# Optimization experiments

Measured on AMD Instinct MI355X. Metric: run time of the kernel, lower is better.

## Reference

```python
import jax, jax.numpy as jnp
import numpy as np

B, N, C = 8, 2048, 256
DK, DV = 64, 256


def setup_inputs() -> dict:
    key = jax.random.key(0)
    kx, kq, kk, kv = jax.random.split(key, 4)
    x = jax.random.normal(kx, (B, N, C), dtype=jnp.float32)
    # Conv1d(kernel=1, bias=False) weights: [out_channels, in_channels]
    Wq = jax.random.normal(kq, (DK, C), dtype=jnp.float32) * (1.0 / np.sqrt(C))
    Wk = jax.random.normal(kk, (DK, C), dtype=jnp.float32) * (1.0 / np.sqrt(C))
    Wv = jax.random.normal(kv, (DV, C), dtype=jnp.float32) * (1.0 / np.sqrt(C))
    return {"x": x, "Wq": Wq, "Wk": Wk, "Wv": Wv}


def reference(x, Wq, Wk, Wv):
    # kernel-size-1 conv == per-point linear projection
    q = jnp.einsum('bnc,dc->bnd', x, Wq)   # [B, N, dk]
    k = jnp.einsum('bnc,dc->bnd', x, Wk)   # [B, N, dk]
    v = jnp.einsum('bnc,dc->bnd', x, Wv)   # [B, N, dv]
    energy = jnp.einsum('bnd,bmd->bnm', q, k)  # [B, N, N] == bmm(q, k^T)
    # offset-attention branch: softmax over dim=1 (column-wise),
    # then renormalize each row to sum to 1
    attention = jax.nn.softmax(energy, axis=1)
    attention = attention / (1e-9 + attention.sum(axis=-1, keepdims=True))
    x_r = jnp.einsum('bnm,bmd->bnd', attention, v)  # [B, N, dv]
    return x_r
```

## Files before the change

### kernel.cpp

```cpp
#include <hip/hip_runtime.h>
#include <hip/hip_bf16.h>

#define BB 8
#define NN 2048
#define CC 256
#define DKK 64
#define DVV 256
#define COFF 60.0f

typedef __attribute__((ext_vector_type(8))) short bf16x8;
typedef __attribute__((ext_vector_type(4))) float f32x4;

#define MFMA16 __builtin_amdgcn_mfma_f32_16x16x32_bf16

static __device__ __forceinline__ unsigned short f2bf(float f) {
    unsigned int u = __float_as_uint(f);
    u += 0x7fffu + ((u >> 16) & 1u);
    return (unsigned short)(u >> 16);
}
static __device__ __forceinline__ float bf2f(unsigned short h) {
    return __uint_as_float(((unsigned int)h) << 16);
}

static __device__ __forceinline__ void g2l16(const unsigned short* g, unsigned short* l) {
    __builtin_amdgcn_global_load_lds(
        (const __attribute__((address_space(1))) void*)g,
        (__attribute__((address_space(3))) void*)l, 16, 0, 0);
}

__global__ void k_wt(const float* __restrict__ Wq, const float* __restrict__ Wk,
                     const float* __restrict__ Wv,
                     unsigned short* __restrict__ Wqkh_s, unsigned short* __restrict__ Wqkl_s,
                     unsigned short* __restrict__ Wvs) {
    int idx = blockIdx.x * 256 + threadIdx.x;
    if (idx >= 384 * 256) return;
    int d = idx >> 8, c = idx & 255;
    float w;
    if (d < 64)       w = Wq[d * 256 + c];
    else if (d < 128) w = Wk[(d - 64) * 256 + c];
    else              w = Wv[(d - 128) * 256 + c];
    unsigned short h = f2bf(w);
    int c8 = c >> 3;
    if (d < 128) {
        int row = d;
        int csw = (((c8 & 24) | ((c8 ^ row) & 7)) << 3) | (c & 7);
        Wqkh_s[row * 256 + csw] = h;
        Wqkl_s[row * 256 + csw] = f2bf(w - bf2f(h));
    } else {
        int row = d - 128;
        int csw = (((c8 & 24) | ((c8 ^ row) & 7)) << 3) | (c & 7);
        Wvs[row * 256 + csw] = h;
    }
}

__global__ __launch_bounds__(256) void k_split(
    const float* __restrict__ x,
    unsigned short* __restrict__ xh, unsigned short* __restrict__ xl) {
    int tid = blockIdx.x * 256 + threadIdx.x;
    const float4* xp = (const float4*)x + tid * 2;
    float4 a = xp[0], b = xp[1];
    float v[8] = {a.x, a.y, a.z, a.w, b.x, b.y, b.z, b.w};
    ushort4 h4[2], l4[2];
    #pragma unroll
    for (int i = 0; i < 8; ++i) {
        unsigned short h = f2bf(v[i]);
        ((unsigned short*)h4)[i] = h;
        ((unsigned short*)l4)[i] = f2bf(v[i] - bf2f(h));
    }
    ((ushort4*)xh)[tid * 2]     = h4[0];
    ((ushort4*)xh)[tid * 2 + 1] = h4[1];
    ((ushort4*)xl)[tid * 2]     = l4[0];
    ((ushort4*)xl)[tid * 2 + 1] = l4[1];
}

__global__ __launch_bounds__(1024) void k_vproj(
    const unsigned short* __restrict__ xh, const unsigned short* __restrict__ Wvs,
    unsigned short* __restrict__ vT)
{
    __shared__ __align__(16) unsigned short Wlds[256 * 256];
    int tid = threadIdx.x;
    int w = tid >> 6, lane = tid & 63;
    int t = lane & 15, qd = lane >> 4;
    int i = w >> 2, j = w & 3;
    int bn0 = blockIdx.x * 64;

    {
        int lr = lane >> 5, lc = (lane & 31) << 3;
        #pragma unroll
        for (int s = 0; s < 8; ++s) {
            int r0 = (w * 8 + s) * 2;
            g2l16(Wvs + (size_t)(r0 + lr) * 256 + lc, &Wlds[0] + (size_t)r0 * 256);
        }
    }

    int bn = bn0 + i * 16 + t;
    int b = bn >> 11, n = bn & 2047;
    bf16x8 bfr[8];
    const unsigned short* bp = xh + (size_t)bn * 256 + qd * 8;
    #pragma unroll
    for (int c = 0; c < 8; ++c) bfr[c] = *(const bf16x8*)(bp + c * 32);

    __syncthreads();

    f32x4 acc[4];
    #pragma unroll
    for (int k = 0; k < 4; ++k) acc[k] = (f32x4){0.f, 0.f, 0.f, 0.f};
    #pragma unroll
    for (int c = 0; c < 8; ++c) {
        #pragma unroll
        for (int k = 0; k < 4; ++k) {
            int d = j * 64 + k * 16 + t;
            int c8 = c * 4 + qd;
            int pos = d * 256 + ((((c8 & 24) | ((c8 ^ t) & 7))) << 3);
            bf16x8 a = *(const bf16x8*)(&Wlds[pos]);
            acc[k] = MFMA16(a, bfr[c], acc[k], 0, 0, 0);
        }
    }
    #pragma unroll
    for (int k = 0; k < 4; ++k) {
        #pragma unroll
        for (int r = 0; r < 4; ++r) {
            int dvd = j * 64 + k * 16 + qd * 4 + r;
            int nsw = (n & ~63) | ((((n >> 3) ^ dvd) & 7) << 3) | (n & 7);
            vT[((size_t)b * 256 + dvd) * 2048 + nsw] = f2bf(acc[k][r]);
        }
    }
}

__global__ __launch_bounds__(1024) void k_qkproj(
    const unsigned short* __restrict__ xh, const unsigned short* __restrict__ xl,
    const unsigned short* __restrict__ Wqkh_s, const unsigned short* __restrict__ Wqkl_s,
    unsigned short* __restrict__ qh, unsigned short* __restrict__ ql,
    unsigned short* __restrict__ kh, unsigned short* __restrict__ kl)
{
    __shared__ __align__(16) unsigned short Wlds[2][128 * 256];
    int tid = threadIdx.x;
    int w = tid >> 6, lane = tid & 63;
    int t = lane & 15, qd = lane >> 4;
    int i = w >> 2, j = w & 3;
    int bn0 = blockIdx.x * 64;

    {
        int lr = lane >> 5, lc = (lane & 31) << 3;
        #pragma unroll
        for (int s = 0; s < 8; ++s) {
            int id = w * 8 + s;
            int plane = id >> 6;
            int r0 = (id & 63) * 2;
            const unsigned short* src = (plane ? Wqkl_s : Wqkh_s) + (size_t)(r0 + lr) * 256 + lc;
            g2l16(src, &Wlds[plane][0] + (size_t)r0 * 256);
        }
    }

    int bn = bn0 + i * 16 + t;
    bf16x8 bh[8], bl[8];
    const unsigned short* bph = xh + (size_t)bn * 256 + qd * 8;
    const unsigned short* bpl = xl + (size_t)bn * 256 + qd * 8;
    #pragma unroll
    for (int c = 0; c < 8; ++c) {
        bh[c] = *(const bf16x8*)(bph + c * 32);
        bl[c] = *(const bf16x8*)(bpl + c * 32);
    }

    __syncthreads();

    f32x4 acc[2];
    acc[0] = (f32x4){0.f, 0.f, 0.f, 0.f};
    acc[1] = (f32x4){0.f, 0.f, 0.f, 0.f};
    #pragma unroll
    for (int c = 0; c < 8; ++c) {
        #pragma unroll
        for (int k = 0; k < 2; ++k) {
            int d = j * 32 + k * 16 + t;
            int c8 = c * 4 + qd;
            int pos = d * 256 + ((((c8 & 24) | ((c8 ^ t) & 7))) << 3);
            bf16x8 ah = *(const bf16x8*)(&Wlds[0][pos]);
            bf16x8 al = *(const bf16x8*)(&Wlds[1][pos]);
            acc[k] = MFMA16(ah, bh[c], acc[k], 0, 0, 0);
            acc[k] = MFMA16(ah, bl[c], acc[k], 0, 0, 0);
            acc[k] = MFMA16(al, bh[c], acc[k], 0, 0, 0);
        }
    }
    #pragma unroll
    for (int k = 0; k < 2; ++k) {
        ushort4 h4, l4;
        #pragma unroll
        for (int r = 0; r < 4; ++r) {
            unsigned short h = f2bf(acc[k][r]);
            ((unsigned short*)&h4)[r] = h;
            ((unsigned short*)&l4)[r] = f2bf(acc[k][r] - bf2f(h));
        }
        int dbase = j * 32 + k * 16 + qd * 4;
        int dd = dbase & 63;
        int sw = ((((dd >> 3) ^ bn) & 7) << 3) | (dd & 7);
        if (dbase < 64) {
            *(ushort4*)(qh + (size_t)bn * 64 + sw) = h4;
            *(ushort4*)(ql + (size_t)bn * 64 + sw) = l4;
        } else {
            *(ushort4*)(kh + (size_t)bn * 64 + sw) = h4;
            *(ushort4*)(kl + (size_t)bn * 64 + sw) = l4;
        }
    }
}

__global__ __launch_bounds__(1024) void k_colsum(
    const unsigned short* __restrict__ qh, const unsigned short* __restrict__ ql,
    const unsigned short* __restrict__ kh, const unsigned short* __restrict__ kl,
    float* __restrict__ cs)
{
    __shared__ __align__(16) unsigned short qbuf[2][2][64 * 64];
    __shared__ float csbuf[4][64];
    int tid = threadIdx.x;
    int w = tid >> 6, lane = tid & 63;
    int t = lane & 15, qd = lane >> 4;
    int b = blockIdx.y, m0 = blockIdx.x * 64;
    int i = w >> 2, j = w & 3;

    int arow = m0 + i * 16 + t;
    int off0 = ((qd ^ (t & 7)) << 3);
    const unsigned short* kbh = kh + ((size_t)b * 2048 + arow) * 64;
    const unsigned short* kbl = kl + ((size_t)b * 2048 + arow) * 64;
    bf16x8 ah0 = *(const bf16x8*)(kbh + off0);
    bf16x8 ah1 = *(const bf16x8*)(kbh + (off0 ^ 32));
    bf16x8 al0 = *(const bf16x8*)(kbl + off0);
    bf16x8 al1 = *(const bf16x8*)(kbl + (off0 ^ 32));

    int lr = lane >> 3, lc = (lane & 7) << 3;
    const unsigned short* qsrc = ((w < 8) ? qh : ql) +
        ((size_t)b * 2048 + (w & 7) * 8 + lr) * 64 + lc;
    unsigned short* qdst = &qbuf[0][w >> 3][(w & 7) * 8 * 64];

#define STAGEQ(bufi, itv) g2l16(qsrc + (size_t)(itv) * (64 * 64), qdst + (bufi) * (2 * 64 * 64))

    float ssum[4] = {0.f, 0.f, 0.f, 0.f};
    STAGEQ(0, 0);
    for (int it = 0; it < 32; ++it) {
        __syncthreads();
        if (it + 1 < 32) STAGEQ((it + 1) & 1, it + 1);
        int cur = it & 1;
        int brow = j * 16 + t;
        const unsigned short* qrh = &qbuf[cur][0][brow * 64];
        const unsigned short* qrl = &qbuf[cur][1][brow * 64];
        bf16x8 bh0 = *(const bf16x8*)(qrh + off0);
        bf16x8 bh1 = *(const bf16x8*)(qrh + (off0 ^ 32));
        bf16x8 bl0 = *(const bf16x8*)(qrl + off0);
        bf16x8 bl1 = *(const bf16x8*)(qrl + (off0 ^ 32));
        f32x4 a0 = {0.f,0.f,0.f,0.f}, a1 = {0.f,0.f,0.f,0.f};
        a0 = MFMA16(ah0, bh0, a0, 0, 0, 0);
        a0 = MFMA16(ah1, bh1, a0, 0, 0, 0);
        a1 = MFMA16(ah0, bl0, a1, 0, 0, 0);
        a1 = MFMA16(ah1, bl1, a1, 0, 0, 0);
        a1 = MFMA16(al0, bh0, a1, 0, 0, 0);
        a1 = MFMA16(al1, bh1, a1, 0, 0, 0);
        #pragma unroll
        for (int r = 0; r < 4; ++r)
            ssum[r] += __expf((a0[r] + a1[r]) - COFF);
    }
#undef STAGEQ

    #pragma unroll
    for (int r = 0; r < 4; ++r) {
        float v = ssum[r];
        v += __shfl_xor(v, 1, 16);
        v += __shfl_xor(v, 2, 16);
        v += __shfl_xor(v, 4, 16);
        v += __shfl_xor(v, 8, 16);
        ssum[r] = v;
    }
    if (t == 0) {
        #pragma unroll
        for (int r = 0; r < 4; ++r) csbuf[j][i * 16 + qd * 4 + r] = ssum[r];
    }
    __syncthreads();
    if (tid < 64)
        cs[(size_t)b * 2048 + m0 + tid] =
            csbuf[0][tid] + csbuf[1][tid] + csbuf[2][tid] + csbuf[3][tid];
}

__global__ __launch_bounds__(1024) void k_attn(
    const unsigned short* __restrict__ qh, const unsigned short* __restrict__ ql,
    const unsigned short* __restrict__ kh, const unsigned short* __restrict__ kl,
    const unsigned short* __restrict__ vT, const float* __restrict__ cs,
    float* __restrict__ out)
{
    __shared__ __align__(16) unsigned short kbuf[2][128 * 64];
    __shared__ __align__(16) unsigned short vbuf[2][256 * 64];
    __shared__ __align__(16) unsigned short pP[64 * 72];
    __shared__ float cs_s[2048];
    __shared__ float rsbuf[4][64];

    int tid = threadIdx.x;
    int w = tid >> 6, lane = tid & 63;
    int t = lane & 15, qd = lane >> 4;
    int b = blockIdx.y;
    int n0 = blockIdx.x * 64;
    int i = w >> 2, j = w & 3;
    int i2 = w >> 3, j8 = w & 7;

    for (int u = tid; u < 2048; u += 1024) cs_s[u] = cs[(size_t)b * 2048 + u];

    int arow_a = n0 + i * 16 + t;
    int offq = ((qd ^ (t & 7)) << 3);
    const unsigned short* qbh = qh + ((size_t)b * 2048 + arow_a) * 64;
    const unsigned short* qbl = ql + ((size_t)b * 2048 + arow_a) * 64;
    bf16x8 ah0 = *(const bf16x8*)(qbh + offq);
    bf16x8 ah1 = *(const bf16x8*)(qbh + (offq ^ 32));
    bf16x8 al0 = *(const bf16x8*)(qbl + offq);
    bf16x8 al1 = *(const bf16x8*)(qbl + (offq ^ 32));

    int lr = lane >> 3, lc = (lane & 7) << 3;
    const unsigned short* vsrc0 = vT + ((size_t)b * 256 + w * 16 + lr) * 2048 + lc;
    const unsigned short* vsrc1 = vT + ((size_t)b * 256 + w * 16 + 8 + lr) * 2048 + lc;
    const unsigned short* karr = (w < 8) ? kh : kl;
    const unsigned short* ksrc = karr + ((size_t)b * 2048 + (w & 7) * 8 + lr) * 64 + lc;
    unsigned short* vdst0 = &vbuf[0][0] + w * 1024;
    unsigned short* vdst1 = vdst0 + 512;
    unsigned short* kdst = &kbuf[0][0] + w * 512;

#define STAGE(bufi, m0s) do { \
        g2l16(vsrc0 + (m0s), vdst0 + (bufi) * 16384); \
        g2l16(vsrc1 + (m0s), vdst1 + (bufi) * 16384); \
        g2l16(ksrc + (size_t)(m0s) * 64, kdst + (bufi) * 8192); \
    } while (0)

    f32x4 accv[2][2];
    accv[0][0] = (f32x4){0.f,0.f,0.f,0.f}; accv[0][1] = (f32x4){0.f,0.f,0.f,0.f};
    accv[1][0] = (f32x4){0.f,0.f,0.f,0.f}; accv[1][1] = (f32x4){0.f,0.f,0.f,0.f};
    float rs[4] = {0.f, 0.f, 0.f, 0.f};

    STAGE(0, 0);

    for (int it = 0; it < 32; ++it) {
        __syncthreads();
        int cur = it & 1;
        int m0 = it * 64;
        {
            int mr = j * 16 + t;
            int off0 = ((qd ^ (t & 7)) << 3);
            const unsigned short* khrow = &kbuf[cur][mr * 64];
            const unsigned short* klrow = &kbuf[cur][(64 + mr) * 64];
            bf16x8 bh0 = *(const bf16x8*)(khrow + off0);
            bf16x8 bh1 = *(const bf16x8*)(khrow + (off0 ^ 32));
            bf16x8 bl0 = *(const bf16x8*)(klrow + off0);
            bf16x8 bl1 = *(const bf16x8*)(klrow + (off0 ^ 32));
            f32x4 s0 = {0.f,0.f,0.f,0.f}, s1 = {0.f,0.f,0.f,0.f};
            s0 = MFMA16(ah0, bh0, s0, 0, 0, 0);
            s0 = MFMA16(ah1, bh1, s0, 0, 0, 0);
            s1 = MFMA16(ah0, bl0, s1, 0, 0, 0);
            s1 = MFMA16(ah1, bl1, s1, 0, 0, 0);
            s1 = MFMA16(al0, bh0, s1, 0, 0, 0);
            s1 = MFMA16(al1, bh1, s1, 0, 0, 0);
            float rcs = 1.0f / cs_s[m0 + j * 16 + t];
            unsigned short* prow = pP + (size_t)(i * 16 + qd * 4) * 72 + j * 16 + t;
            #pragma unroll
            for (int r = 0; r < 4; ++r) {
                float p = __expf((s0[r] + s1[r]) - COFF) * rcs;
                rs[r] += p;
                prow[r * 72] = f2bf(p);
            }
        }
        if (it + 1 < 32) STAGE((it + 1) & 1, m0 + 64);
        __syncthreads();
        {
            const unsigned short* vb = &vbuf[cur][0];
            #pragma unroll
            for (int c = 0; c < 2; ++c) {
                bf16x8 pa0 = *(const bf16x8*)(pP + (size_t)((2*i2 + 0) * 16 + t) * 72 + c * 32 + qd * 8);
                bf16x8 pa1 = *(const bf16x8*)(pP + (size_t)((2*i2 + 1) * 16 + t) * 72 + c * 32 + qd * 8);
                int ch = (((c * 4 + qd) ^ (t & 7)) << 3);
                bf16x8 vb0 = *(const bf16x8*)(vb + ((2*j8 + 0) * 16 + t) * 64 + ch);
                bf16x8 vb1 = *(const bf16x8*)(vb + ((2*j8 + 1) * 16 + t) * 64 + ch);
                accv[0][0] = MFMA16(pa0, vb0, accv[0][0], 0, 0, 0);
                accv[0][1] = MFMA16(pa0, vb1, accv[0][1], 0, 0, 0);
                accv[1][0] = MFMA16(pa1, vb0, accv[1][0], 0, 0, 0);
                accv[1][1] = MFMA16(pa1, vb1, accv[1][1], 0, 0, 0);
            }
        }
    }
#undef STAGE

    #pragma unroll
    for (int r = 0; r < 4; ++r) {
        float v = rs[r];
        v += __shfl_xor(v, 1, 16);
        v += __shfl_xor(v, 2, 16);
        v += __shfl_xor(v, 4, 16);
        v += __shfl_xor(v, 8, 16);
        rs[r] = v;
    }
    if (t == 0) {
        #pragma unroll
        for (int r = 0; r < 4; ++r) rsbuf[j][i * 16 + qd * 4 + r] = rs[r];
    }
    __syncthreads();

    #pragma unroll
    for (int s2 = 0; s2 < 2; ++s2) {
        #pragma unroll
        for (int r = 0; r < 4; ++r) {
            int nl = (2 * i2 + s2) * 16 + qd * 4 + r;
            float tot = rsbuf[0][nl] + rsbuf[1][nl] + rsbuf[2][nl] + rsbuf[3][nl];
            float sc = 1.0f / (1e-9f + tot);
            size_t orow = ((size_t)b * 2048 + n0 + nl) * 256;
            out[orow + (2 * j8 + 0) * 16 + t] = accv[s2][0][r] * sc;
            out[orow + (2 * j8 + 1) * 16 + t] = accv[s2][1][r] * sc;
        }
    }
}

extern "C" void kernel_launch(void* const* d_in, const int* in_sizes, int n_in,
                              void* d_out, int out_size, void* d_ws, size_t ws_size,
                              hipStream_t stream) {
    (void)in_sizes; (void)n_in; (void)out_size; (void)ws_size;
    const float* x  = (const float*)d_in[0];
    const float* Wq = (const float*)d_in[1];
    const float* Wk = (const float*)d_in[2];
    const float* Wv = (const float*)d_in[3];
    float* out = (float*)d_out;

    char* ws = (char*)d_ws;
    size_t off = 0;
    unsigned short* Wqkh_s = (unsigned short*)(ws + off); off += (size_t)128 * 256 * 2;
    unsigned short* Wqkl_s = (unsigned short*)(ws + off); off += (size_t)128 * 256 * 2;
    unsigned short* Wvs    = (unsigned short*)(ws + off); off += (size_t)256 * 256 * 2;
    unsigned short* xh = (unsigned short*)(ws + off); off += (size_t)BB * NN * CC * 2;
    unsigned short* xl = (unsigned short*)(ws + off); off += (size_t)BB * NN * CC * 2;
    unsigned short* qh = (unsigned short*)(ws + off); off += (size_t)BB * NN * DKK * 2;
    unsigned short* ql = (unsigned short*)(ws + off); off += (size_t)BB * NN * DKK * 2;
    unsigned short* kh = (unsigned short*)(ws + off); off += (size_t)BB * NN * DKK * 2;
    unsigned short* kl = (unsigned short*)(ws + off); off += (size_t)BB * NN * DKK * 2;
    unsigned short* vT = (unsigned short*)(ws + off); off += (size_t)BB * DVV * NN * 2;
    float* cs = (float*)(ws + off);                   off += (size_t)BB * NN * 4;

    hipLaunchKernelGGL(k_wt,     dim3(384),         dim3(256),  0, stream, Wq, Wk, Wv, Wqkh_s, Wqkl_s, Wvs);
    hipLaunchKernelGGL(k_split,  dim3(2048),        dim3(256),  0, stream, x, xh, xl);
    hipLaunchKernelGGL(k_vproj,  dim3(256),         dim3(1024), 0, stream, xh, Wvs, vT);
    hipLaunchKernelGGL(k_qkproj, dim3(256),         dim3(1024), 0, stream, xh, xl, Wqkh_s, Wqkl_s, qh, ql, kh, kl);
    hipLaunchKernelGGL(k_colsum, dim3(NN / 64, BB), dim3(1024), 0, stream, qh, ql, kh, kl, cs);
    hipLaunchKernelGGL(k_attn,   dim3(NN / 64, BB), dim3(1024), 0, stream, qh, ql, kh, kl, vT, cs, out);
}
```

Baseline: 167.5 us.

## Fuse x split and Q/K/V projections into one kernel, prefetch attention stage earlier

Removes the separate x hi/lo split kernel and merges the V and QK projection kernels into one launch with two roles chosen by blockIdx.y. Each block converts fp32 x to bf16 hi/lo in registers, so the xh/xl workspace round trip and two launches go away. In the attention kernel, the next tile's async stage is issued before the QK/softmax compute instead of after it, giving more overlap. In exchange, V blocks now also read fp32 x and compute an unused lo split, and the earlier prefetch depends on the buffer sync order still being correct.

Result: slower. 205.5 us (+22.7%).

```diff
diff --git a/kernel.cpp b/kernel.cpp
--- a/kernel.cpp
+++ b/kernel.cpp
@@ -53,28 +53,12 @@
     }
 }
 
-__global__ __launch_bounds__(256) void k_split(
+__global__ __launch_bounds__(1024) void k_proj(
     const float* __restrict__ x,
-    unsigned short* __restrict__ xh, unsigned short* __restrict__ xl) {
-    int tid = blockIdx.x * 256 + threadIdx.x;
-    const float4* xp = (const float4*)x + tid * 2;
-    float4 a = xp[0], b = xp[1];
-    float v[8] = {a.x, a.y, a.z, a.w, b.x, b.y, b.z, b.w};
-    ushort4 h4[2], l4[2];
-    #pragma unroll
-    for (int i = 0; i < 8; ++i) {
-        unsigned short h = f2bf(v[i]);
-        ((unsigned short*)h4)[i] = h;
-        ((unsigned short*)l4)[i] = f2bf(v[i] - bf2f(h));
-    }
-    ((ushort4*)xh)[tid * 2]     = h4[0];
-    ((ushort4*)xh)[tid * 2 + 1] = h4[1];
-    ((ushort4*)xl)[tid * 2]     = l4[0];
-    ((ushort4*)xl)[tid * 2 + 1] = l4[1];
-}
-
-__global__ __launch_bounds__(1024) void k_vproj(
-    const unsigned short* __restrict__ xh, const unsigned short* __restrict__ Wvs,
+    const unsigned short* __restrict__ Wqkh_s, const unsigned short* __restrict__ Wqkl_s,
+    const unsigned short* __restrict__ Wvs,
+    unsigned short* __restrict__ qh, unsigned short* __restrict__ ql,
+    unsigned short* __restrict__ kh, unsigned short* __restrict__ kl,
     unsigned short* __restrict__ vT)
 {
     __shared__ __align__(16) unsigned short Wlds[256 * 256];
@@ -83,122 +67,109 @@
     int t = lane & 15, qd = lane >> 4;
     int i = w >> 2, j = w & 3;
     int bn0 = blockIdx.x * 64;
+    int role_qk = (blockIdx.y == 0);
 
     {
         int lr = lane >> 5, lc = (lane & 31) << 3;
-        #pragma unroll
-        for (int s = 0; s < 8; ++s) {
-            int r0 = (w * 8 + s) * 2;
-            g2l16(Wvs + (size_t)(r0 + lr) * 256 + lc, &Wlds[0] + (size_t)r0 * 256);
+        if (role_qk) {
+            #pragma unroll
+            for (int s = 0; s < 8; ++s) {
+                int id = w * 8 + s;
+                int plane = id >> 6;
+                int r0 = (id & 63) * 2;
+                const unsigned short* src = (plane ? Wqkl_s : Wqkh_s) + (size_t)(r0 + lr) * 256 + lc;
+                g2l16(src, &Wlds[0] + ((size_t)plane * 128 + r0) * 256);
+            }
+        } else {
+            #pragma unroll
+            for (int s = 0; s < 8; ++s) {
+                int r0 = (w * 8 + s) * 2;
+                g2l16(Wvs + (size_t)(r0 + lr) * 256 + lc, &Wlds[0] + (size_t)r0 * 256);
+            }
         }
     }
 
     int bn = bn0 + i * 16 + t;
     int b = bn >> 11, n = bn & 2047;
-    bf16x8 bfr[8];
-    const unsigned short* bp = xh + (size_t)bn * 256 + qd * 8;
-    #pragma unroll
-    for (int c = 0; c < 8; ++c) bfr[c] = *(const bf16x8*)(bp + c * 32);
-
-    __syncthreads();
-
-    f32x4 acc[4];
-    #pragma unroll
-    for (int k = 0; k < 4; ++k) acc[k] = (f32x4){0.f, 0.f, 0.f, 0.f};
+
+    bf16x8 bh[8], bl[8];
+    const float* xf = x + (size_t)bn * 256 + qd * 8;
     #pragma unroll
     for (int c = 0; c < 8; ++c) {
+        float4 f0 = *(const float4*)(xf + c * 32);
+        float4 f1 = *(const float4*)(xf + c * 32 + 4);
+        float v[8] = {f0.x, f0.y, f0.z, f0.w, f1.x, f1.y, f1.z, f1.w};
+        #pragma unroll
+        for (int e = 0; e < 8; ++e) {
+            unsigned short h = f2bf(v[e]);
+            bh[c][e] = (short)h;
+            bl[c][e] = (short)f2bf(v[e] - bf2f(h));
+        }
+    }
+
+    __syncthreads();
+
+    if (role_qk) {
+        f32x4 acc[2];
+        acc[0] = (f32x4){0.f, 0.f, 0.f, 0.f};
+        acc[1] = (f32x4){0.f, 0.f, 0.f, 0.f};
+        #pragma unroll
+        for (int c = 0; c < 8; ++c) {
+            #pragma unroll
+            for (int k = 0; k < 2; ++k) {
+                int d = j * 32 + k * 16 + t;
+                int c8 = c * 4 + qd;
+                int pos = d * 256 + ((((c8 & 24) | ((c8 ^ t) & 7))) << 3);
+                bf16x8 ah = *(const bf16x8*)(&Wlds[pos]);
+                bf16x8 al = *(const bf16x8*)(&Wlds[128 * 256 + pos]);
+                acc[k] = MFMA16(ah, bh[c], acc[k], 0, 0, 0);
+                acc[k] = MFMA16(ah, bl[c], acc[k], 0, 0, 0);
+                acc[k] = MFMA16(al, bh[c], acc[k], 0, 0, 0);
+            }
+        }
+        #pragma unroll
+        for (int k = 0; k < 2; ++k) {
+            ushort4 h4, l4;
+            #pragma unroll
+            for (int r = 0; r < 4; ++r) {
+                unsigned short h = f2bf(acc[k][r]);
+                ((unsigned short*)&h4)[r] = h;
+                ((unsigned short*)&l4)[r] = f2bf(acc[k][r] - bf2f(h));
+            }
+            int dbase = j * 32 + k * 16 + qd * 4;
+            int dd = dbase & 63;
+            int sw = ((((dd >> 3) ^ bn) & 7) << 3) | (dd & 7);
+            if (dbase < 64) {
+                *(ushort4*)(qh + (size_t)bn * 64 + sw) = h4;
+                *(ushort4*)(ql + (size_t)bn * 64 + sw) = l4;
+            } else {
+                *(ushort4*)(kh + (size_t)bn * 64 + sw) = h4;
+                *(ushort4*)(kl + (size_t)bn * 64 + sw) = l4;
+            }
+        }
+    } else {
+        f32x4 acc[4];
+        #pragma unroll
+        for (int k = 0; k < 4; ++k) acc[k] = (f32x4){0.f, 0.f, 0.f, 0.f};
+        #pragma unroll
+        for (int c = 0; c < 8; ++c) {
+            #pragma unroll
+            for (int k = 0; k < 4; ++k) {
+                int d = j * 64 + k * 16 + t;
+                int c8 = c * 4 + qd;
+                int pos = d * 256 + ((((c8 & 24) | ((c8 ^ t) & 7))) << 3);
+                bf16x8 a = *(const bf16x8*)(&Wlds[pos]);
+                acc[k] = MFMA16(a, bh[c], acc[k], 0, 0, 0);
+            }
+        }
         #pragma unroll
         for (int k = 0; k < 4; ++k) {
-            int d = j * 64 + k * 16 + t;
-            int c8 = c * 4 + qd;
-            int pos = d * 256 + ((((c8 & 24) | ((c8 ^ t) & 7))) << 3);
-            bf16x8 a = *(const bf16x8*)(&Wlds[pos]);
-            acc[k] = MFMA16(a, bfr[c], acc[k], 0, 0, 0);
-        }
-    }
-    #pragma unroll
-    for (int k = 0; k < 4; ++k) {
-        #pragma unroll
-        for (int r = 0; r < 4; ++r) {
-            int dvd = j * 64 + k * 16 + qd * 4 + r;
-            int nsw = (n & ~63) | ((((n >> 3) ^ dvd) & 7) << 3) | (n & 7);
-            vT[((size_t)b * 256 + dvd) * 2048 + nsw] = f2bf(acc[k][r]);
-        }
-    }
-}
-
-__global__ __launch_bounds__(1024) void k_qkproj(
-    const unsigned short* __restrict__ xh, const unsigned short* __restrict__ xl,
-    const unsigned short* __restrict__ Wqkh_s, const unsigned short* __restrict__ Wqkl_s,
-    unsigned short* __restrict__ qh, unsigned short* __restrict__ ql,
-    unsigned short* __restrict__ kh, unsigned short* __restrict__ kl)
-{
-    __shared__ __align__(16) unsigned short Wlds[2][128 * 256];
-    int tid = threadIdx.x;
-    int w = tid >> 6, lane = tid & 63;
-    int t = lane & 15, qd = lane >> 4;
-    int i = w >> 2, j = w & 3;
-    int bn0 = blockIdx.x * 64;
-
-    {
-        int lr = lane >> 5, lc = (lane & 31) << 3;
-        #pragma unroll
-        for (int s = 0; s < 8; ++s) {
-            int id = w * 8 + s;
-            int plane = id >> 6;
-            int r0 = (id & 63) * 2;
-            const unsigned short* src = (plane ? Wqkl_s : Wqkh_s) + (size_t)(r0 + lr) * 256 + lc;
-            g2l16(src, &Wlds[plane][0] + (size_t)r0 * 256);
-        }
-    }
-
-    int bn = bn0 + i * 16 + t;
-    bf16x8 bh[8], bl[8];
-    const unsigned short* bph = xh + (size_t)bn * 256 + qd * 8;
-    const unsigned short* bpl = xl + (size_t)bn * 256 + qd * 8;
-    #pragma unroll
-    for (int c = 0; c < 8; ++c) {
-        bh[c] = *(const bf16x8*)(bph + c * 32);
-        bl[c] = *(const bf16x8*)(bpl + c * 32);
-    }
-
-    __syncthreads();
-
-    f32x4 acc[2];
-    acc[0] = (f32x4){0.f, 0.f, 0.f, 0.f};
-    acc[1] = (f32x4){0.f, 0.f, 0.f, 0.f};
-    #pragma unroll
-    for (int c = 0; c < 8; ++c) {
-        #pragma unroll
-        for (int k = 0; k < 2; ++k) {
-            int d = j * 32 + k * 16 + t;
-            int c8 = c * 4 + qd;
-            int pos = d * 256 + ((((c8 & 24) | ((c8 ^ t) & 7))) << 3);
-            bf16x8 ah = *(const bf16x8*)(&Wlds[0][pos]);
-            bf16x8 al = *(const bf16x8*)(&Wlds[1][pos]);
-            acc[k] = MFMA16(ah, bh[c], acc[k], 0, 0, 0);
-            acc[k] = MFMA16(ah, bl[c], acc[k], 0, 0, 0);
-            acc[k] = MFMA16(al, bh[c], acc[k], 0, 0, 0);
-        }
-    }
-    #pragma unroll
-    for (int k = 0; k < 2; ++k) {
-        ushort4 h4, l4;
-        #pragma unroll
-        for (int r = 0; r < 4; ++r) {
-            unsigned short h = f2bf(acc[k][r]);
-            ((unsigned short*)&h4)[r] = h;
-            ((unsigned short*)&l4)[r] = f2bf(acc[k][r] - bf2f(h));
-        }
-        int dbase = j * 32 + k * 16 + qd * 4;
-        int dd = dbase & 63;
-        int sw = ((((dd >> 3) ^ bn) & 7) << 3) | (dd & 7);
-        if (dbase < 64) {
-            *(ushort4*)(qh + (size_t)bn * 64 + sw) = h4;
-            *(ushort4*)(ql + (size_t)bn * 64 + sw) = l4;
-        } else {
-            *(ushort4*)(kh + (size_t)bn * 64 + sw) = h4;
-            *(ushort4*)(kl + (size_t)bn * 64 + sw) = l4;
+            #pragma unroll
+            for (int r = 0; r < 4; ++r) {
+                int dvd = j * 64 + k * 16 + qd * 4 + r;
+                int nsw = (n & ~63) | ((((n >> 3) ^ dvd) & 7) << 3) | (n & 7);
+                vT[((size_t)b * 256 + dvd) * 2048 + nsw] = f2bf(acc[k][r]);
+            }
         }
     }
 }
@@ -334,6 +305,7 @@
         __syncthreads();
         int cur = it & 1;
         int m0 = it * 64;
+        if (it + 1 < 32) STAGE(cur ^ 1, m0 + 64);
         {
             int mr = j * 16 + t;
             int off0 = ((qd ^ (t & 7)) << 3);
@@ -359,7 +331,6 @@
                 prow[r * 72] = f2bf(p);
             }
         }
-        if (it + 1 < 32) STAGE((it + 1) & 1, m0 + 64);
         __syncthreads();
         {
             const unsigned short* vb = &vbuf[cur][0];
@@ -423,8 +394,6 @@
     unsigned short* Wqkh_s = (unsigned short*)(ws + off); off += (size_t)128 * 256 * 2;
     unsigned short* Wqkl_s = (unsigned short*)(ws + off); off += (size_t)128 * 256 * 2;
     unsigned short* Wvs    = (unsigned short*)(ws + off); off += (size_t)256 * 256 * 2;
-    unsigned short* xh = (unsigned short*)(ws + off); off += (size_t)BB * NN * CC * 2;
-    unsigned short* xl = (unsigned short*)(ws + off); off += (size_t)BB * NN * CC * 2;
     unsigned short* qh = (unsigned short*)(ws + off); off += (size_t)BB * NN * DKK * 2;
     unsigned short* ql = (unsigned short*)(ws + off); off += (size_t)BB * NN * DKK * 2;
     unsigned short* kh = (unsigned short*)(ws + off); off += (size_t)BB * NN * DKK * 2;
@@ -433,9 +402,7 @@
     float* cs = (float*)(ws + off);                   off += (size_t)BB * NN * 4;
 
     hipLaunchKernelGGL(k_wt,     dim3(384),         dim3(256),  0, stream, Wq, Wk, Wv, Wqkh_s, Wqkl_s, Wvs);
-    hipLaunchKernelGGL(k_split,  dim3(2048),        dim3(256),  0, stream, x, xh, xl);
-    hipLaunchKernelGGL(k_vproj,  dim3(256),         dim3(1024), 0, stream, xh, Wvs, vT);
-    hipLaunchKernelGGL(k_qkproj, dim3(256),         dim3(1024), 0, stream, xh, xl, Wqkh_s, Wqkl_s, qh, ql, kh, kl);
+    hipLaunchKernelGGL(k_proj,   dim3(256, 2),      dim3(1024), 0, stream, x, Wqkh_s, Wqkl_s, Wvs, qh, ql, kh, kl, vT);
     hipLaunchKernelGGL(k_colsum, dim3(NN / 64, BB), dim3(1024), 0, stream, qh, ql, kh, kl, cs);
     hipLaunchKernelGGL(k_attn,   dim3(NN / 64, BB), dim3(1024), 0, stream, qh, ql, kh, kl, vT, cs, out);
 }
```

## Halve attention row tile and read V directly from global memory

Applied to the files above, without the earlier changes.

The attention kernel now handles 32 query rows per block with 512 threads, doubling the block count. V is no longer staged through LDS double buffers. Each wave loads its V fragments straight from global memory (through cache) inside the PV loop. This cuts LDS use and copy traffic so more blocks can be resident. The trade-off is that V and K are re-read by twice as many blocks, and the PV loop now waits on global-load latency without software prefetch.

Result: slower. 201.0 us (+20.0%).

```diff
diff --git a/kernel.cpp b/kernel.cpp
--- a/kernel.cpp
+++ b/kernel.cpp
@@ -277,27 +277,26 @@
             csbuf[0][tid] + csbuf[1][tid] + csbuf[2][tid] + csbuf[3][tid];
 }
 
-__global__ __launch_bounds__(1024) void k_attn(
+__global__ __launch_bounds__(512) void k_attn(
     const unsigned short* __restrict__ qh, const unsigned short* __restrict__ ql,
     const unsigned short* __restrict__ kh, const unsigned short* __restrict__ kl,
     const unsigned short* __restrict__ vT, const float* __restrict__ cs,
     float* __restrict__ out)
 {
     __shared__ __align__(16) unsigned short kbuf[2][128 * 64];
-    __shared__ __align__(16) unsigned short vbuf[2][256 * 64];
-    __shared__ __align__(16) unsigned short pP[64 * 72];
+    __shared__ __align__(16) unsigned short pP[32 * 72];
     __shared__ float cs_s[2048];
-    __shared__ float rsbuf[4][64];
+    __shared__ float rsbuf[4][32];
 
     int tid = threadIdx.x;
     int w = tid >> 6, lane = tid & 63;
     int t = lane & 15, qd = lane >> 4;
     int b = blockIdx.y;
-    int n0 = blockIdx.x * 64;
+    int n0 = blockIdx.x * 32;
     int i = w >> 2, j = w & 3;
-    int i2 = w >> 3, j8 = w & 7;
-
-    for (int u = tid; u < 2048; u += 1024) cs_s[u] = cs[(size_t)b * 2048 + u];
+    int i2 = w & 1, j4 = w >> 1;
+
+    for (int u = tid; u < 2048; u += 512) cs_s[u] = cs[(size_t)b * 2048 + u];
 
     int arow_a = n0 + i * 16 + t;
     int offq = ((qd ^ (t & 7)) << 3);
@@ -309,23 +308,21 @@
     bf16x8 al1 = *(const bf16x8*)(qbl + (offq ^ 32));
 
     int lr = lane >> 3, lc = (lane & 7) << 3;
-    const unsigned short* vsrc0 = vT + ((size_t)b * 256 + w * 16 + lr) * 2048 + lc;
-    const unsigned short* vsrc1 = vT + ((size_t)b * 256 + w * 16 + 8 + lr) * 2048 + lc;
-    const unsigned short* karr = (w < 8) ? kh : kl;
-    const unsigned short* ksrc = karr + ((size_t)b * 2048 + (w & 7) * 8 + lr) * 64 + lc;
-    unsigned short* vdst0 = &vbuf[0][0] + w * 1024;
-    unsigned short* vdst1 = vdst0 + 512;
-    unsigned short* kdst = &kbuf[0][0] + w * 512;
+    const unsigned short* ksrc0 = ((w * 2 + 0) >> 3 ? kl : kh) +
+        ((size_t)b * 2048 + ((w * 2 + 0) & 7) * 8 + lr) * 64 + lc;
+    const unsigned short* ksrc1 = ((w * 2 + 1) >> 3 ? kl : kh) +
+        ((size_t)b * 2048 + ((w * 2 + 1) & 7) * 8 + lr) * 64 + lc;
+    unsigned short* kdst0 = &kbuf[0][0] + ((((w * 2 + 0) >> 3) * 64 + ((w * 2 + 0) & 7) * 8) * 64);
+    unsigned short* kdst1 = &kbuf[0][0] + ((((w * 2 + 1) >> 3) * 64 + ((w * 2 + 1) & 7) * 8) * 64);
 
 #define STAGE(bufi, m0s) do { \
-        g2l16(vsrc0 + (m0s), vdst0 + (bufi) * 16384); \
-        g2l16(vsrc1 + (m0s), vdst1 + (bufi) * 16384); \
-        g2l16(ksrc + (size_t)(m0s) * 64, kdst + (bufi) * 8192); \
+        g2l16(ksrc0 + (size_t)(m0s) * 64, kdst0 + (bufi) * 8192); \
+        g2l16(ksrc1 + (size_t)(m0s) * 64, kdst1 + (bufi) * 8192); \
     } while (0)
 
-    f32x4 accv[2][2];
-    accv[0][0] = (f32x4){0.f,0.f,0.f,0.f}; accv[0][1] = (f32x4){0.f,0.f,0.f,0.f};
-    accv[1][0] = (f32x4){0.f,0.f,0.f,0.f}; accv[1][1] = (f32x4){0.f,0.f,0.f,0.f};
+    f32x4 acc[4];
+    #pragma unroll
+    for (int ds = 0; ds < 4; ++ds) acc[ds] = (f32x4){0.f, 0.f, 0.f, 0.f};
     float rs[4] = {0.f, 0.f, 0.f, 0.f};
 
     STAGE(0, 0);
@@ -359,22 +356,21 @@
                 prow[r * 72] = f2bf(p);
             }
         }
-        if (it + 1 < 32) STAGE((it + 1) & 1, m0 + 64);
+        if (it + 1 < 32) STAGE(cur ^ 1, m0 + 64);
         __syncthreads();
-        {
-            const unsigned short* vb = &vbuf[cur][0];
+        #pragma unroll
+        for (int c = 0; c < 2; ++c) {
+            bf16x8 pa = *(const bf16x8*)(pP + (size_t)(i2 * 16 + t) * 72 + c * 32 + qd * 8);
+            int ch = (((c * 4 + qd) ^ (t & 7)) << 3);
+            bf16x8 vbf[4];
             #pragma unroll
-            for (int c = 0; c < 2; ++c) {
-                bf16x8 pa0 = *(const bf16x8*)(pP + (size_t)((2*i2 + 0) * 16 + t) * 72 + c * 32 + qd * 8);
-                bf16x8 pa1 = *(const bf16x8*)(pP + (size_t)((2*i2 + 1) * 16 + t) * 72 + c * 32 + qd * 8);
-                int ch = (((c * 4 + qd) ^ (t & 7)) << 3);
-                bf16x8 vb0 = *(const bf16x8*)(vb + ((2*j8 + 0) * 16 + t) * 64 + ch);
-                bf16x8 vb1 = *(const bf16x8*)(vb + ((2*j8 + 1) * 16 + t) * 64 + ch);
-                accv[0][0] = MFMA16(pa0, vb0, accv[0][0], 0, 0, 0);
-                accv[0][1] = MFMA16(pa0, vb1, accv[0][1], 0, 0, 0);
-                accv[1][0] = MFMA16(pa1, vb0, accv[1][0], 0, 0, 0);
-                accv[1][1] = MFMA16(pa1, vb1, accv[1][1], 0, 0, 0);
+            for (int ds = 0; ds < 4; ++ds) {
+                int vrow = j4 * 64 + ds * 16 + t;
+                vbf[ds] = *(const bf16x8*)(vT + ((size_t)b * 256 + vrow) * 2048 + m0 + ch);
             }
+            #pragma unroll
+            for (int ds = 0; ds < 4; ++ds)
+                acc[ds] = MFMA16(pa, vbf[ds], acc[ds], 0, 0, 0);
         }
     }
 #undef STAGE
@@ -395,16 +391,14 @@
     __syncthreads();
 
     #pragma unroll
-    for (int s2 = 0; s2 < 2; ++s2) {
-        #pragma unroll
-        for (int r = 0; r < 4; ++r) {
-            int nl = (2 * i2 + s2) * 16 + qd * 4 + r;
-            float tot = rsbuf[0][nl] + rsbuf[1][nl] + rsbuf[2][nl] + rsbuf[3][nl];
-            float sc = 1.0f / (1e-9f + tot);
-            size_t orow = ((size_t)b * 2048 + n0 + nl) * 256;
-            out[orow + (2 * j8 + 0) * 16 + t] = accv[s2][0][r] * sc;
-            out[orow + (2 * j8 + 1) * 16 + t] = accv[s2][1][r] * sc;
-        }
+    for (int r = 0; r < 4; ++r) {
+        int nl = i2 * 16 + qd * 4 + r;
+        float tot = rsbuf[0][nl] + rsbuf[1][nl] + rsbuf[2][nl] + rsbuf[3][nl];
+        float sc = 1.0f / (1e-9f + tot);
+        size_t orow = ((size_t)b * 2048 + n0 + nl) * 256;
+        #pragma unroll
+        for (int ds = 0; ds < 4; ++ds)
+            out[orow + j4 * 64 + ds * 16 + t] = acc[ds][r] * sc;
     }
 }
 
@@ -437,5 +431,5 @@
     hipLaunchKernelGGL(k_vproj,  dim3(256),         dim3(1024), 0, stream, xh, Wvs, vT);
     hipLaunchKernelGGL(k_qkproj, dim3(256),         dim3(1024), 0, stream, xh, xl, Wqkh_s, Wqkl_s, qh, ql, kh, kl);
     hipLaunchKernelGGL(k_colsum, dim3(NN / 64, BB), dim3(1024), 0, stream, qh, ql, kh, kl, cs);
-    hipLaunchKernelGGL(k_attn,   dim3(NN / 64, BB), dim3(1024), 0, stream, qh, ql, kh, kl, vT, cs, out);
-}
+    hipLaunchKernelGGL(k_attn,   dim3(NN / 32, BB), dim3(512),  0, stream, qh, ql, kh, kl, vT, cs, out);
+}
```
